# Kernel tuning notes

Hardware: AMD Instinct MI355X
Metric: run time of the kernel (lower is better)

The kernel has to match this reference:

```python
import jax, jax.numpy as jnp
import numpy as np

IN_F = 256
OUT_F = 512
DEG = 3
BATCH = 2048


def setup_inputs() -> dict:
    key = jax.random.key(0)
    k_x, k_p, k_q, k_w = jax.random.split(key, 4)
    x = jax.random.normal(k_x, (BATCH, IN_F), dtype=jnp.float32)
    P_coef = jax.random.normal(k_p, (OUT_F, IN_F, DEG + 1), dtype=jnp.float32) * 0.1
    Q_coef = jax.random.normal(k_q, (OUT_F, IN_F, DEG), dtype=jnp.float32) * 0.1
    # reset_parameters(): constant term of P zeroed, constant of Q set to 1
    P_coef = P_coef.at[:, :, 0].set(0.0)
    Q_coef = Q_coef.at[:, :, 0].set(1.0)
    # xavier_uniform for base_weight
    limit = float(np.sqrt(6.0 / (IN_F + OUT_F)))
    base_weight = jax.random.uniform(k_w, (OUT_F, IN_F), dtype=jnp.float32,
                                     minval=-limit, maxval=limit)
    base_bias = jnp.zeros((OUT_F,), dtype=jnp.float32)
    return {"x": x, "P_coef": P_coef, "Q_coef": Q_coef,
            "base_weight": base_weight, "base_bias": base_bias}


def reference(x, P_coef, Q_coef, base_weight, base_bias):
    # x: (B, I). Powers x^0..x^DEG -> (B, I, DEG+1)
    exps = jnp.arange(DEG + 1, dtype=x.dtype)
    x_powers = x[..., None] ** exps  # (B, I, P)
    # P[b,i,o] = sum_p P_coef[o,i,p] * x[b,i]^p
    P = jnp.einsum('oip,bip->bio', P_coef, x_powers)
    # Q uses powers x^1..x^DEG
    Q = 1.0 + jnp.einsum('oip,bip->bio', Q_coef, x_powers[:, :, 1:])
    rational = P / (Q + 1e-6)          # (B, I, O)
    rational_output = rational.sum(axis=1)  # (B, O)
    base_output = x @ base_weight.T + base_bias  # (B, O)
    return base_output + rational_output
```

## Files before the change

kernel.cpp:

```cpp
#include <hip/hip_runtime.h>

constexpr int IN_F  = 256;
constexpr int OUT_F = 512;
constexpr int BATCH = 2048;

__global__ __launch_bounds__(256) void prep_pack8_kernel(
    const float* __restrict__ p, const float* __restrict__ q,
    const float* __restrict__ w, float4* __restrict__ pk, int n) {
    int t = blockIdx.x * 256 + threadIdx.x;
    if (t < n) {
        pk[2 * t]     = make_float4(p[4 * t], p[4 * t + 1], p[4 * t + 2], p[4 * t + 3]);
        pk[2 * t + 1] = make_float4(q[3 * t], q[3 * t + 1], q[3 * t + 2], w[t]);
    }
}

__global__ __launch_bounds__(256) void prep_x3_kernel(
    const float* __restrict__ x, float* __restrict__ x3, int n) {
    int t = blockIdx.x * 256 + threadIdx.x;
    if (t < n) {
        const double xd = (double)x[t];
        x3[t] = (float)(xd * xd * xd);
    }
}

template <int MODE>
__global__ __launch_bounds__(256, 8) void kan_kernel(
    const float*  __restrict__ x,
    const float4* __restrict__ Pc,
    const float*  __restrict__ Qc,
    const float4* __restrict__ PK,
    const float*  __restrict__ X3,
    const float*  __restrict__ W,
    const float*  __restrict__ bias,
    float* __restrict__ out)
{
#pragma clang fp contract(off)
    const int lane  = threadIdx.x & 63;
    const int wave  = __builtin_amdgcn_readfirstlane(threadIdx.x >> 6);
    const int b     = blockIdx.x * 64 + lane;
    const int o0    = blockIdx.y * 8;
    const int ibase = wave * 64;

    float acc[8] = {0.f, 0.f, 0.f, 0.f, 0.f, 0.f, 0.f, 0.f};
    const float* xrow  = x + (size_t)b * IN_F + ibase;
    const float* x3row = (MODE == 2) ? (X3 + (size_t)b * IN_F + ibase) : nullptr;

    for (int ic = 0; ic < 64; ic += 4) {
        const float4 xq = *reinterpret_cast<const float4*>(xrow + ic);
        float x1[4] = {xq.x, xq.y, xq.z, xq.w};
        float x2[4], x3[4];
        if (MODE == 2) {
            const float4 x3q = *reinterpret_cast<const float4*>(x3row + ic);
            x3[0] = x3q.x; x3[1] = x3q.y; x3[2] = x3q.z; x3[3] = x3q.w;
#pragma unroll
            for (int j = 0; j < 4; ++j) x2[j] = x1[j] * x1[j];
        } else {
#pragma unroll
            for (int j = 0; j < 4; ++j) {
                x2[j] = x1[j] * x1[j];
                const double xd = (double)x1[j];
                x3[j] = (float)(xd * xd * xd);
            }
        }
        const int rowi = ibase + ic;
#pragma unroll
        for (int oo = 0; oo < 8; ++oo) {
            const int rowbase = (o0 + oo) * IN_F + rowi;
#pragma unroll
            for (int j = 0; j < 4; ++j) {
                float p0, p1, p2, p3, q1, q2, q3, wv;
                if (MODE >= 1) {
                    const float4 pa = PK[2 * (rowbase + j)];
                    const float4 pb = PK[2 * (rowbase + j) + 1];
                    p0 = pa.x; p1 = pa.y; p2 = pa.z; p3 = pa.w;
                    q1 = pb.x; q2 = pb.y; q3 = pb.z; wv = pb.w;
                } else {
                    const float4 pc = Pc[rowbase + j];
                    const float* qp = Qc + (size_t)(rowbase + j) * 3;
                    p0 = pc.x; p1 = pc.y; p2 = pc.z; p3 = pc.w;
                    q1 = qp[0]; q2 = qp[1]; q3 = qp[2];
                    wv = W[rowbase + j];
                }
                float t = q1 * x1[j];
                t = fmaf(q2, x2[j], t);
                t = fmaf(q3, x3[j], t);
                float Qv = 1.0f + t;
                float Qp = Qv + 1e-6f;
                float s = fmaf(p1, x1[j], p0);
                s = fmaf(p2, x2[j], s);
                s = fmaf(p3, x3[j], s);
                const float r = __builtin_amdgcn_rcpf(Qp);
                acc[oo] = fmaf(s, r, acc[oo]);
                acc[oo] = fmaf(wv, x1[j], acc[oo]);
            }
        }
    }

    __shared__ float red[4 * 64 * 8];
    float4* dst = reinterpret_cast<float4*>(&red[(wave * 64 + lane) * 8]);
    dst[0] = make_float4(acc[0], acc[1], acc[2], acc[3]);
    dst[1] = make_float4(acc[4], acc[5], acc[6], acc[7]);
    __syncthreads();

#pragma unroll
    for (int k = 0; k < 2; ++k) {
        const int idx = threadIdx.x + k * 256;
        float s = red[idx] + red[512 + idx];
        s = s + red[1024 + idx];
        s = s + red[1536 + idx];
        const int bb = idx >> 3, o = idx & 7;
        s = s + bias[o0 + o];
        out[(size_t)(blockIdx.x * 64 + bb) * OUT_F + o0 + o] = s;
    }
}

extern "C" void kernel_launch(void* const* d_in, const int* in_sizes, int n_in,
                              void* d_out, int out_size, void* d_ws, size_t ws_size,
                              hipStream_t stream) {
    const float* x    = (const float*)d_in[0];
    const float* Pc   = (const float*)d_in[1];
    const float* Qc   = (const float*)d_in[2];
    const float* W    = (const float*)d_in[3];
    const float* bias = (const float*)d_in[4];
    float* out = (float*)d_out;

    const int n  = OUT_F * IN_F;
    const int nx = BATCH * IN_F;
    const size_t pk_bytes = (size_t)n * 32;
    dim3 grid(BATCH / 64, OUT_F / 8);

    if (ws_size >= pk_bytes + (size_t)nx * sizeof(float)) {
        float4* pk = (float4*)d_ws;
        float*  x3 = (float*)((char*)d_ws + pk_bytes);
        prep_pack8_kernel<<<(n + 255) / 256, 256, 0, stream>>>(Pc, Qc, W, pk, n);
        prep_x3_kernel<<<(nx + 255) / 256, 256, 0, stream>>>(x, x3, nx);
        kan_kernel<2><<<grid, 256, 0, stream>>>(
            x, (const float4*)Pc, Qc, pk, x3, W, bias, out);
    } else if (ws_size >= pk_bytes) {
        float4* pk = (float4*)d_ws;
        prep_pack8_kernel<<<(n + 255) / 256, 256, 0, stream>>>(Pc, Qc, W, pk, n);
        kan_kernel<1><<<grid, 256, 0, stream>>>(
            x, (const float4*)Pc, Qc, pk, nullptr, W, bias, out);
    } else {
        kan_kernel<0><<<grid, 256, 0, stream>>>(
            x, (const float4*)Pc, Qc, nullptr, nullptr, W, bias, out);
    }
}
```

Baseline: 108.5 us.

## Stage packed coefficients through double-buffered LDS per wave with register prefetch

```diff
diff --git a/kernel.cpp b/kernel.cpp
--- a/kernel.cpp
+++ b/kernel.cpp
@@ -45,58 +45,104 @@
     const float* xrow  = x + (size_t)b * IN_F + ibase;
     const float* x3row = (MODE == 2) ? (X3 + (size_t)b * IN_F + ibase) : nullptr;
 
-    for (int ic = 0; ic < 64; ic += 4) {
-        const float4 xq = *reinterpret_cast<const float4*>(xrow + ic);
-        float x1[4] = {xq.x, xq.y, xq.z, xq.w};
-        float x2[4], x3[4];
-        if (MODE == 2) {
-            const float4 x3q = *reinterpret_cast<const float4*>(x3row + ic);
-            x3[0] = x3q.x; x3[1] = x3q.y; x3[2] = x3q.z; x3[3] = x3q.w;
+    __shared__ float4 cbuf[4][2][64];
+    __shared__ float  red[4 * 64 * 8];
+
+    if (MODE == 2) {
+        const int c   = lane >> 3;
+        const int sub = lane & 7;
+        const size_t gbase = 2 * ((size_t)(o0 + c) * IN_F) + sub;
+
+        float4 st = PK[gbase + 2 * (size_t)(ibase + 0)];
+        cbuf[wave][0][lane] = st;
+        st = PK[gbase + 2 * (size_t)(ibase + 4)];
+        float4 xq  = *reinterpret_cast<const float4*>(xrow);
+        float4 x3q = *reinterpret_cast<const float4*>(x3row);
+
+        for (int k = 0; k < 16; ++k) {
+            const int par = k & 1;
+            if (k < 15) {
+                cbuf[wave][par ^ 1][lane] = st;
+                if (k < 14)
+                    st = PK[gbase + 2 * (size_t)(ibase + 4 * (k + 2))];
+            }
+            float x1[4]  = {xq.x, xq.y, xq.z, xq.w};
+            float x3v[4] = {x3q.x, x3q.y, x3q.z, x3q.w};
+            if (k < 15) {
+                xq  = *reinterpret_cast<const float4*>(xrow  + 4 * (k + 1));
+                x3q = *reinterpret_cast<const float4*>(x3row + 4 * (k + 1));
+            }
+            float x2[4];
 #pragma unroll
             for (int j = 0; j < 4; ++j) x2[j] = x1[j] * x1[j];
-        } else {
+
+            const float4* cb = cbuf[wave][par];
+#pragma unroll
+            for (int oo = 0; oo < 8; ++oo) {
+#pragma unroll
+                for (int j = 0; j < 4; ++j) {
+                    const float4 pa = cb[(oo * 4 + j) * 2];
+                    const float4 pb = cb[(oo * 4 + j) * 2 + 1];
+                    float t = pb.x * x1[j];
+                    t = fmaf(pb.y, x2[j], t);
+                    t = fmaf(pb.z, x3v[j], t);
+                    float Qv = 1.0f + t;
+                    float Qp = Qv + 1e-6f;
+                    float s = fmaf(pa.y, x1[j], pa.x);
+                    s = fmaf(pa.z, x2[j], s);
+                    s = fmaf(pa.w, x3v[j], s);
+                    const float r = __builtin_amdgcn_rcpf(Qp);
+                    acc[oo] = fmaf(s, r, acc[oo]);
+                    acc[oo] = fmaf(pb.w, x1[j], acc[oo]);
+                }
+            }
+        }
+    } else {
+        for (int ic = 0; ic < 64; ic += 4) {
+            const float4 xq = *reinterpret_cast<const float4*>(xrow + ic);
+            float x1[4] = {xq.x, xq.y, xq.z, xq.w};
+            float x2[4], x3v[4];
 #pragma unroll
             for (int j = 0; j < 4; ++j) {
                 x2[j] = x1[j] * x1[j];
                 const double xd = (double)x1[j];
-                x3[j] = (float)(xd * xd * xd);
+                x3v[j] = (float)(xd * xd * xd);
             }
-        }
-        const int rowi = ibase + ic;
+            const int rowi = ibase + ic;
 #pragma unroll
-        for (int oo = 0; oo < 8; ++oo) {
-            const int rowbase = (o0 + oo) * IN_F + rowi;
+            for (int oo = 0; oo < 8; ++oo) {
+                const int rowbase = (o0 + oo) * IN_F + rowi;
 #pragma unroll
-            for (int j = 0; j < 4; ++j) {
-                float p0, p1, p2, p3, q1, q2, q3, wv;
-                if (MODE >= 1) {
-                    const float4 pa = PK[2 * (rowbase + j)];
-                    const float4 pb = PK[2 * (rowbase + j) + 1];
-                    p0 = pa.x; p1 = pa.y; p2 = pa.z; p3 = pa.w;
-                    q1 = pb.x; q2 = pb.y; q3 = pb.z; wv = pb.w;
-                } else {
-                    const float4 pc = Pc[rowbase + j];
-                    const float* qp = Qc + (size_t)(rowbase + j) * 3;
-                    p0 = pc.x; p1 = pc.y; p2 = pc.z; p3 = pc.w;
-                    q1 = qp[0]; q2 = qp[1]; q3 = qp[2];
-                    wv = W[rowbase + j];
+                for (int j = 0; j < 4; ++j) {
+                    float p0, p1, p2, p3, q1, q2, q3, wv;
+                    if (MODE == 1) {
+                        const float4 pa = PK[2 * (size_t)(rowbase + j)];
+                        const float4 pb = PK[2 * (size_t)(rowbase + j) + 1];
+                        p0 = pa.x; p1 = pa.y; p2 = pa.z; p3 = pa.w;
+                        q1 = pb.x; q2 = pb.y; q3 = pb.z; wv = pb.w;
+                    } else {
+                        const float4 pc = Pc[rowbase + j];
+                        const float* qp = Qc + (size_t)(rowbase + j) * 3;
+                        p0 = pc.x; p1 = pc.y; p2 = pc.z; p3 = pc.w;
+                        q1 = qp[0]; q2 = qp[1]; q3 = qp[2];
+                        wv = W[rowbase + j];
+                    }
+                    float t = q1 * x1[j];
+                    t = fmaf(q2, x2[j], t);
+                    t = fmaf(q3, x3v[j], t);
+                    float Qv = 1.0f + t;
+                    float Qp = Qv + 1e-6f;
+                    float s = fmaf(p1, x1[j], p0);
+                    s = fmaf(p2, x2[j], s);
+                    s = fmaf(p3, x3v[j], s);
+                    const float r = __builtin_amdgcn_rcpf(Qp);
+                    acc[oo] = fmaf(s, r, acc[oo]);
+                    acc[oo] = fmaf(wv, x1[j], acc[oo]);
                 }
-                float t = q1 * x1[j];
-                t = fmaf(q2, x2[j], t);
-                t = fmaf(q3, x3[j], t);
-                float Qv = 1.0f + t;
-                float Qp = Qv + 1e-6f;
-                float s = fmaf(p1, x1[j], p0);
-                s = fmaf(p2, x2[j], s);
-                s = fmaf(p3, x3[j], s);
-                const float r = __builtin_amdgcn_rcpf(Qp);
-                acc[oo] = fmaf(s, r, acc[oo]);
-                acc[oo] = fmaf(wv, x1[j], acc[oo]);
             }
         }
     }
 
-    __shared__ float red[4 * 64 * 8];
     float4* dst = reinterpret_cast<float4*>(&red[(wave * 64 + lane) * 8]);
     dst[0] = make_float4(acc[0], acc[1], acc[2], acc[3]);
     dst[1] = make_float4(acc[4], acc[5], acc[6], acc[7]);
```

Result: slower. 191.6 us (+76.6%).
